# Performance work log

Hardware: AMD Instinct MI355X
Metric: run time of the kernel (lower is better)

## Reference

```python
import jax, jax.numpy as jnp
import numpy as np

N = 40000          # spots (nodes)
G = 3000           # genes (input features)
C = 20             # num_classes
E = N * 16         # edges (avg degree 16)


def _uniform(key, shape, stdv):
    return jax.random.uniform(key, shape, jnp.float32, -stdv, stdv)


def _linear_params(key, n_in, n_out):
    # torch Linear default init: U(-1/sqrt(in), 1/sqrt(in)); stored as [in, out]
    k1, k2 = jax.random.split(key)
    s = 1.0 / np.sqrt(n_in)
    return _uniform(k1, (n_in, n_out), s), _uniform(k2, (n_out,), s)


def setup_inputs() -> dict:
    key = jax.random.key(0)
    ks = jax.random.split(key, 32)
    x = jax.random.normal(ks[0], (N, G), jnp.float32)
    adj_rows = jax.random.randint(ks[1], (E,), 0, N, jnp.int32)
    adj_cols = jax.random.randint(ks[2], (E,), 0, N, jnp.int32)
    adj_vals = jax.random.uniform(ks[3], (E,), jnp.float32)

    # GCN weights: GraphConvolution init U(-1/sqrt(out), 1/sqrt(out)), no bias
    def gcn_w(k, fi, fo):
        return _uniform(k, (fi, fo), 1.0 / np.sqrt(fo))

    inp = {
        "x": x, "adj_rows": adj_rows, "adj_cols": adj_cols, "adj_vals": adj_vals,
        "W1": gcn_w(ks[4], G, 512), "W2": gcn_w(ks[5], 512, 256),
        "W3": gcn_w(ks[6], 256, 128), "W4": gcn_w(ks[7], 128, 128),
        "W5": gcn_w(ks[8], 128, C),
    }
    # AE linear layers
    for name, (fi, fo), k in [
        ("enc1", (G, 512), ks[9]), ("enc2", (512, 256), ks[10]),
        ("enc3", (256, 128), ks[11]), ("zl", (128, 128), ks[12]),
        ("dec1", (128, 128), ks[13]), ("dec2", (128, 256), ks[14]),
        ("dec3", (256, 512), ks[15]), ("xbar", (512, G), ks[16]),
    ]:
        w, b = _linear_params(k, fi, fo)
        inp[name + "_w"], inp[name + "_b"] = w, b
    # Attention projection vectors (Linear(in_size, 1, bias=False))
    inp["a1"] = _uniform(ks[17], (512,), 1.0 / np.sqrt(512))
    inp["a2"] = _uniform(ks[18], (256,), 1.0 / np.sqrt(256))
    inp["a3"] = _uniform(ks[19], (128,), 1.0 / np.sqrt(128))
    inp["a4"] = _uniform(ks[20], (128,), 1.0 / np.sqrt(128))
    inp["scale"] = jax.random.normal(ks[21], (G,), jnp.float32)
    inp["additive"] = jax.random.normal(ks[22], (G,), jnp.float32)
    return inp


def _spmm(rows, cols, vals, dense, n):
    # out[r] = sum_e vals[e] * dense[cols[e]] for rows[e]==r  (sparse [n,n] @ dense)
    return jax.ops.segment_sum(vals[:, None] * dense[cols], rows, num_segments=n)


def _gcn(x, rows, cols, vals, W, n, active=True):
    out = _spmm(rows, cols, vals, x @ W, n)
    return jax.nn.relu(out) if active else out


def _attn(h, t, a):
    # stack two [N,D] branches, softmax over the branch axis, weighted sum
    z = jnp.stack([h, t], axis=1)           # [N,2,D]
    w = jnp.einsum('nbd,d->nb', z, a)        # [N,2]
    beta = jax.nn.softmax(w, axis=1)
    return jnp.einsum('nb,nbd->nd', beta, z)


def reference(x, adj_rows, adj_cols, adj_vals,
              W1, W2, W3, W4, W5,
              enc1_w, enc1_b, enc2_w, enc2_b, enc3_w, enc3_b, zl_w, zl_b,
              dec1_w, dec1_b, dec2_w, dec2_b, dec3_w, dec3_b, xbar_w, xbar_b,
              a1, a2, a3, a4, scale, additive):
    n = x.shape[0]
    # autoencoder
    t1 = jax.nn.relu(x @ enc1_w + enc1_b)
    t2 = jax.nn.relu(t1 @ enc2_w + enc2_b)
    t3 = jax.nn.relu(t2 @ enc3_w + enc3_b)
    z = t3 @ zl_w + zl_b
    d1 = jax.nn.relu(z @ dec1_w + dec1_b)
    d2 = jax.nn.relu(d1 @ dec2_w + dec2_b)
    d3 = jax.nn.relu(d2 @ dec3_w + dec3_b)
    x_bar = d3 @ xbar_w + xbar_b
    # GCN stack with attention-fused AE skip connections
    h = _gcn(x, adj_rows, adj_cols, adj_vals, W1, n)
    emb = _attn(h, t1, a1)
    h = _gcn(emb, adj_rows, adj_cols, adj_vals, W2, n)
    emb = _attn(h, t2, a2)
    h = _gcn(emb, adj_rows, adj_cols, adj_vals, W3, n)
    emb = _attn(h, t3, a3)
    h = _gcn(emb, adj_rows, adj_cols, adj_vals, W4, n)
    emb = _attn(h, z, a4)
    output = _gcn(emb, adj_rows, adj_cols, adj_vals, W5, n, active=False)
    return output, x_bar, jax.nn.sigmoid(scale), jnp.exp(additive)
```

## Files before the change

### kernel.cpp

```cpp
#include <hip/hip_runtime.h>
#include <cmath>

typedef unsigned short u16;
typedef unsigned int u32;
typedef __attribute__((ext_vector_type(8))) short short8;
typedef __attribute__((ext_vector_type(4))) short short4v;
typedef __attribute__((ext_vector_type(4))) float f32x4;

__device__ __forceinline__ float bf2f(u16 h) {
  union { u32 u; float f; } v; v.u = ((u32)h) << 16; return v.f;
}
__device__ __forceinline__ u16 f2bf(float f) {
  union { float f; u32 u; } v; v.f = f;
  u32 u = v.u;
  u32 r = (u + 0x7FFFu + ((u >> 16) & 1u)) >> 16;
  return (u16)r;
}

__global__ void convx_kernel(const float* __restrict__ x, u16* __restrict__ A0) {
  int idx = blockIdx.x * 256 + threadIdx.x;
  int r = blockIdx.y;
  if (idx >= 752) return;
  short4v o;
  if (r < 40000 && idx < 750) {
    float4 v = *(const float4*)(x + (size_t)r * 3000 + idx * 4);
    o[0] = (short)f2bf(v.x); o[1] = (short)f2bf(v.y);
    o[2] = (short)f2bf(v.z); o[3] = (short)f2bf(v.w);
  } else {
    o[0] = 0; o[1] = 0; o[2] = 0; o[3] = 0;
  }
  *(short4v*)(A0 + (size_t)r * 3008 + idx * 4) = o;
}

__global__ void convw_kernel(const float* __restrict__ W, u16* __restrict__ Wt,
                             int K, int N, int Kp) {
  int k = blockIdx.x * 256 + threadIdx.x;
  int n = blockIdx.y;
  if (k >= Kp) return;
  float v = (k < K && n < N) ? W[(size_t)k * N + n] : 0.f;
  Wt[(size_t)n * Kp + k] = f2bf(v);
}

__global__ void zero_kernel(int* p, int n) {
  int i = blockIdx.x * 256 + threadIdx.x;
  if (i < n) p[i] = 0;
}
__global__ void count_kernel(const int* __restrict__ rows, int* __restrict__ counts, int E) {
  int i = blockIdx.x * 256 + threadIdx.x;
  if (i < E) atomicAdd(&counts[rows[i]], 1);
}
__global__ __launch_bounds__(1024) void scan_kernel(const int* __restrict__ counts,
                                                    int* __restrict__ rowptr,
                                                    int* __restrict__ cursor, int n) {
  __shared__ int buf[1024];
  __shared__ int carry_s;
  int tid = threadIdx.x;
  if (tid == 0) carry_s = 0;
  __syncthreads();
  for (int base = 0; base < n; base += 1024) {
    int i = base + tid;
    int v = (i < n) ? counts[i] : 0;
    buf[tid] = v;
    __syncthreads();
    for (int off = 1; off < 1024; off <<= 1) {
      int tv = (tid >= off) ? buf[tid - off] : 0;
      __syncthreads();
      buf[tid] += tv;
      __syncthreads();
    }
    int incl = buf[tid];
    int carry = carry_s;
    if (i < n) { int ex = carry + incl - v; rowptr[i] = ex; cursor[i] = ex; }
    __syncthreads();
    if (tid == 1023) carry_s = carry + incl;
    __syncthreads();
  }
  if (tid == 0) rowptr[n] = carry_s;
}
__global__ void scatter_kernel(const int* __restrict__ rows, const int* __restrict__ cols,
                               const float* __restrict__ vals, int* __restrict__ cursor,
                               int* __restrict__ cols_s, float* __restrict__ vals_s, int E) {
  int i = blockIdx.x * 256 + threadIdx.x;
  if (i < E) {
    int r = rows[i];
    int p = atomicAdd(&cursor[r], 1);
    cols_s[p] = cols[i];
    vals_s[p] = vals[i];
  }
}

#define BM 128
#define BN 128
#define BK 32

template <bool BIAS, bool RELU, bool OUTBF16, int CH>
__global__ __launch_bounds__(256, 2) void gemm_bf16(
    const u16* __restrict__ A, int lda, const u16* __restrict__ Bt, int ldb,
    void* __restrict__ C1, int ldc,
    const float* __restrict__ bias, int M, int Nreal, int K, int MT, int NT) {
  __shared__ __align__(16) u16 As[2][BM * BK];
  __shared__ __align__(16) u16 Bs[2][BN * BK];
  const int lin = blockIdx.x;
  const int per = CH * NT;
  const int g = lin / per;
  const int r0 = lin - g * per;
  const int bx0 = g * CH;
  const int cw = min(CH, MT - bx0);
  const int bx = bx0 + r0 % cw;
  const int by = r0 / cw;

  const int tid = threadIdx.x;
  const int lane = tid & 63;
  const int wave = tid >> 6;
  const int mblk = bx * BM;
  const int nblk = by * BN;
  const int wm = (wave & 1) * 64;
  const int wn = (wave >> 1) * 64;
  const int ml = lane & 15;
  const int kg = lane >> 4;

  f32x4 acc[4][4];
#pragma unroll
  for (int i = 0; i < 4; ++i)
#pragma unroll
    for (int j = 0; j < 4; ++j) acc[i][j] = (f32x4)(0.f);

  const int nk = K / BK;
  const int sr = tid >> 2;
  const int sc = (tid & 3) * 8;
  const u16* gA0 = A + (size_t)(mblk + sr) * lda + sc;
  const u16* gA1 = A + (size_t)(mblk + sr + 64) * lda + sc;
  const u16* gB0 = Bt + (size_t)(nblk + sr) * ldb + sc;
  const u16* gB1 = Bt + (size_t)(nblk + sr + 64) * ldb + sc;

  auto stage = [&](int buf, int kt) {
    const int ko = kt * BK;
    u16* lA = &As[buf][0] + wave * 512;
    u16* lB = &Bs[buf][0] + wave * 512;
    __builtin_amdgcn_global_load_lds((const void*)(gA0 + ko), (void*)lA, 16, 0, 0);
    __builtin_amdgcn_global_load_lds((const void*)(gA1 + ko), (void*)(lA + 2048), 16, 0, 0);
    __builtin_amdgcn_global_load_lds((const void*)(gB0 + ko), (void*)lB, 16, 0, 0);
    __builtin_amdgcn_global_load_lds((const void*)(gB1 + ko), (void*)(lB + 2048), 16, 0, 0);
  };

  stage(0, 0);
  asm volatile("s_waitcnt vmcnt(0)" ::: "memory");
  __syncthreads();

  int cur = 0;
  for (int kt = 0; kt < nk; ++kt) {
    if (kt + 1 < nk) stage(cur ^ 1, kt + 1);
    short8 af[4], bfr[4];
#pragma unroll
    for (int i = 0; i < 4; ++i) {
      af[i] = *(const short8*)&As[cur][(wm + i * 16 + ml) * BK + kg * 8];
      bfr[i] = *(const short8*)&Bs[cur][(wn + i * 16 + ml) * BK + kg * 8];
    }
#pragma unroll
    for (int i = 0; i < 4; ++i)
#pragma unroll
      for (int j = 0; j < 4; ++j)
        acc[i][j] = __builtin_amdgcn_mfma_f32_16x16x32_bf16(af[i], bfr[j], acc[i][j], 0, 0, 0);
    asm volatile("s_waitcnt vmcnt(0)" ::: "memory");
    __syncthreads();
    cur ^= 1;
  }

#pragma unroll
  for (int i = 0; i < 4; ++i) {
    const int row0 = mblk + wm + i * 16 + kg * 4;
#pragma unroll
    for (int j = 0; j < 4; ++j) {
      const int col = nblk + wn + j * 16 + ml;
      if (col < Nreal) {
        float bv = BIAS ? bias[col] : 0.f;
#pragma unroll
        for (int r = 0; r < 4; ++r) {
          const int row = row0 + r;
          if (row < M) {
            float v = acc[i][j][r] + bv;
            if (RELU) v = fmaxf(v, 0.f);
            if (OUTBF16)
              ((u16*)C1)[(size_t)row * ldc + col] = f2bf(v);
            else
              ((float*)C1)[(size_t)row * ldc + col] = v;
          }
        }
      }
    }
  }
}

template <bool BIAS, bool RELU, bool OUTBF16, bool SPLIT>
__global__ __launch_bounds__(512, 1) void gemm256v2(
    const u16* __restrict__ A, int lda, const u16* __restrict__ Bt, int ldb,
    void* __restrict__ C1, void* __restrict__ C2, int ldc,
    const float* __restrict__ bias, int M, int Nreal, int K, int MT, int NT) {
  __shared__ __align__(16) u16 smem[(2 * 128 + 2 * 256) * 64];
  u16* As0 = smem;
  u16* Bs0 = smem + 2 * 128 * 64;
  const int tid = threadIdx.x;
  const int lane = tid & 63;
  const int wave = tid >> 6;
  const int wm = wave >> 2;
  const int wn = wave & 3;
  const int ml = lane & 15;
  const int kg = lane >> 4;

  const int grp = blockIdx.x / (8 * NT);
  const int rr = blockIdx.x % (8 * NT);
  const int nb = min(8, MT - grp * 8);
  const int bx = grp * 8 + rr % nb;
  const int by = rr / nb;
  const int mblk = bx * 128;
  const int nblk = by * 256;

  f32x4 acc[4][4];
#pragma unroll
  for (int i = 0; i < 4; ++i)
#pragma unroll
    for (int j = 0; j < 4; ++j) acc[i][j] = (f32x4)(0.f);

  const int srow = tid >> 3;
  const int clog = (tid & 7) ^ (srow & 7);
  const size_t abase = (size_t)(mblk + srow) * lda + clog * 8;
  const size_t bbase = (size_t)(nblk + srow) * ldb + clog * 8;
  const int NKT = K / 64;

  auto stageA = [&](int d, int kt, int h) {
    u16* dst = As0 + d * 8192 + h * 4096 + wave * 512;
    const u16* src = A + abase + (size_t)h * 64 * lda + kt * 64;
    __builtin_amdgcn_global_load_lds((const void*)src, (void*)dst, 16, 0, 0);
  };
  auto stageB = [&](int d, int kt, int h) {
    u16* dst = Bs0 + d * 16384 + h * 4096 + wave * 512;
    const u16* src = Bt + bbase + (size_t)h * 64 * ldb + kt * 64;
    __builtin_amdgcn_global_load_lds((const void*)src, (void*)dst, 16, 0, 0);
  };
  auto stageAll = [&](int d, int kt) {
    stageB(d, kt, 0); stageB(d, kt, 1); stageB(d, kt, 2); stageB(d, kt, 3);
    stageA(d, kt, 0); stageA(d, kt, 1);
  };
  auto readA = [&](int d, int im, int kk) -> short8 {
    const int r = wm * 64 + im * 16 + ml;
    const int ch = (kk * 4 + kg) ^ (r & 7);
    return *(const short8*)&As0[d * 8192 + r * 64 + ch * 8];
  };
  auto readB = [&](int d, int j, int kk) -> short8 {
    const int r = wn * 64 + j * 16 + ml;
    const int ch = (kk * 4 + kg) ^ (r & 7);
    return *(const short8*)&Bs0[d * 16384 + r * 64 + ch * 8];
  };

  stageAll(0, 0);
  __syncthreads();

  for (int kt = 0; kt < NKT; ++kt) {
    const int d = kt & 1;
    if (kt + 1 < NKT) stageAll(d ^ 1, kt + 1);

    short8 b[4][2];
#pragma unroll
    for (int j = 0; j < 4; ++j) { b[j][0] = readB(d, j, 0); b[j][1] = readB(d, j, 1); }
    short8 aC0k0 = readA(d, 0, 0), aC0k1 = readA(d, 0, 1);
    short8 aC1k0 = readA(d, 1, 0), aC1k1 = readA(d, 1, 1);
#pragma unroll
    for (int q = 0; q < 2; ++q) {
      short8 aN0k0, aN0k1, aN1k0, aN1k1;
      if (q == 0) {
        aN0k0 = readA(d, 2, 0); aN0k1 = readA(d, 2, 1);
        aN1k0 = readA(d, 3, 0); aN1k1 = readA(d, 3, 1);
      }
      __builtin_amdgcn_s_setprio(1);
#pragma unroll
      for (int j = 0; j < 4; ++j) {
        acc[2 * q][j]     = __builtin_amdgcn_mfma_f32_16x16x32_bf16(aC0k0, b[j][0], acc[2 * q][j], 0, 0, 0);
        acc[2 * q + 1][j] = __builtin_amdgcn_mfma_f32_16x16x32_bf16(aC1k0, b[j][0], acc[2 * q + 1][j], 0, 0, 0);
      }
#pragma unroll
      for (int j = 0; j < 4; ++j) {
        acc[2 * q][j]     = __builtin_amdgcn_mfma_f32_16x16x32_bf16(aC0k1, b[j][1], acc[2 * q][j], 0, 0, 0);
        acc[2 * q + 1][j] = __builtin_amdgcn_mfma_f32_16x16x32_bf16(aC1k1, b[j][1], acc[2 * q + 1][j], 0, 0, 0);
      }
      __builtin_amdgcn_s_setprio(0);
      if (q == 0) { aC0k0 = aN0k0; aC0k1 = aN0k1; aC1k0 = aN1k0; aC1k1 = aN1k1; }
    }
    __syncthreads();
  }

  if (!SPLIT && !OUTBF16) {
    float* ep = (float*)smem;
    const int ES = 260;
    const int scol = nblk + lane * 4;
    float bv0 = 0.f, bv1 = 0.f, bv2 = 0.f, bv3 = 0.f;
    if (BIAS) {
      if (scol + 3 < Nreal) {
        float4 b4 = *(const float4*)(bias + scol);
        bv0 = b4.x; bv1 = b4.y; bv2 = b4.z; bv3 = b4.w;
      } else {
        if (scol + 0 < Nreal) bv0 = bias[scol + 0];
        if (scol + 1 < Nreal) bv1 = bias[scol + 1];
        if (scol + 2 < Nreal) bv2 = bias[scol + 2];
        if (scol + 3 < Nreal) bv3 = bias[scol + 3];
      }
    }
#pragma unroll
    for (int p = 0; p < 2; ++p) {
      if (p) __syncthreads();
#pragma unroll
      for (int il = 0; il < 2; ++il) {
        const int i = 2 * p + il;
        const int lrow0 = wm * 32 + il * 16 + kg * 4;
#pragma unroll
        for (int j = 0; j < 4; ++j) {
          const int colL = wn * 64 + j * 16 + ml;
#pragma unroll
          for (int r = 0; r < 4; ++r) ep[(lrow0 + r) * ES + colL] = acc[i][j][r];
        }
      }
      __syncthreads();
#pragma unroll
      for (int it = 0; it < 8; ++it) {
        const int lrow = wave * 8 + it;
        const int grow = mblk + p * 32 + (lrow & 31) + (lrow >> 5) * 64;
        if (grow < M) {
          float v0 = ep[lrow * ES + lane * 4 + 0] + bv0;
          float v1 = ep[lrow * ES + lane * 4 + 1] + bv1;
          float v2 = ep[lrow * ES + lane * 4 + 2] + bv2;
          float v3 = ep[lrow * ES + lane * 4 + 3] + bv3;
          if (RELU) {
            v0 = fmaxf(v0, 0.f); v1 = fmaxf(v1, 0.f);
            v2 = fmaxf(v2, 0.f); v3 = fmaxf(v3, 0.f);
          }
          float* dst = (float*)C1 + (size_t)grow * ldc + scol;
          if (scol + 3 < Nreal) {
            float4 v; v.x = v0; v.y = v1; v.z = v2; v.w = v3;
            *(float4*)dst = v;
          } else {
            if (scol + 0 < Nreal) dst[0] = v0;
            if (scol + 1 < Nreal) dst[1] = v1;
            if (scol + 2 < Nreal) dst[2] = v2;
            if (scol + 3 < Nreal) dst[3] = v3;
          }
        }
      }
    }
    return;
  }

  const int crow0 = mblk + wm * 64;
  const int ccol0 = nblk + wn * 64;
#pragma unroll
  for (int i = 0; i < 4; ++i) {
    const int row0 = crow0 + i * 16 + kg * 4;
#pragma unroll
    for (int j = 0; j < 4; ++j) {
      const int col = ccol0 + j * 16 + ml;
      if (SPLIT) {
        const bool second = (nblk >= 512);
        const float bv = second ? 0.f : bias[col];
#pragma unroll
        for (int r = 0; r < 4; ++r) {
          const int row = row0 + r;
          if (row < M) {
            float v = acc[i][j][r] + bv;
            if (!second) v = fmaxf(v, 0.f);
            u16* dst = second ? (u16*)C2 : (u16*)C1;
            dst[(size_t)row * 512 + (second ? col - 512 : col)] = f2bf(v);
          }
        }
      } else if (col < Nreal) {
        const float bv = BIAS ? bias[col] : 0.f;
#pragma unroll
        for (int r = 0; r < 4; ++r) {
          const int row = row0 + r;
          if (row < M) {
            float v = acc[i][j][r] + bv;
            if (RELU) v = fmaxf(v, 0.f);
            if (OUTBF16)
              ((u16*)C1)[(size_t)row * ldc + col] = f2bf(v);
            else
              ((float*)C1)[(size_t)row * ldc + col] = v;
          }
        }
      }
    }
  }
}

template <int D>
__global__ __launch_bounds__(256) void spmm_attn(const int* __restrict__ rowptr,
                                                 const int* __restrict__ colidx,
                                                 const float* __restrict__ vals,
                                                 const u16* __restrict__ X,
                                                 const u16* __restrict__ T,
                                                 const float* __restrict__ a,
                                                 u16* __restrict__ emb) {
  constexpr int VE = D / 64;
  const int wave = threadIdx.x >> 6, lane = threadIdx.x & 63;
  const int row = blockIdx.x * 4 + wave;
  const int co = lane * VE;
  float h[VE];
#pragma unroll
  for (int j = 0; j < VE; ++j) h[j] = 0.f;
  const int s = rowptr[row], e = rowptr[row + 1];
  for (int i = s; i < e; ++i) {
    const int c = colidx[i];
    const float v = vals[i];
    const u16* xr = X + (size_t)c * D + co;
    if constexpr (VE == 8) {
      short8 x8 = *(const short8*)xr;
#pragma unroll
      for (int j = 0; j < 8; ++j) h[j] += v * bf2f((u16)x8[j]);
    } else if constexpr (VE == 4) {
      short4v x4 = *(const short4v*)xr;
#pragma unroll
      for (int j = 0; j < 4; ++j) h[j] += v * bf2f((u16)x4[j]);
    } else {
      u32 x2 = *(const u32*)xr;
      h[0] += v * bf2f((u16)(x2 & 0xffffu));
      h[1] += v * bf2f((u16)(x2 >> 16));
    }
  }
#pragma unroll
  for (int j = 0; j < VE; ++j) h[j] = fmaxf(h[j], 0.f);

  float tv[VE];
  const u16* tr = T + (size_t)row * D + co;
  if constexpr (VE == 8) {
    short8 t8 = *(const short8*)tr;
#pragma unroll
    for (int j = 0; j < 8; ++j) tv[j] = bf2f((u16)t8[j]);
  } else if constexpr (VE == 4) {
    short4v t4 = *(const short4v*)tr;
#pragma unroll
    for (int j = 0; j < 4; ++j) tv[j] = bf2f((u16)t4[j]);
  } else {
    u32 t2 = *(const u32*)tr;
    tv[0] = bf2f((u16)(t2 & 0xffffu)); tv[1] = bf2f((u16)(t2 >> 16));
  }

  float wh = 0.f, wt = 0.f;
#pragma unroll
  for (int j = 0; j < VE; ++j) {
    float av = a[co + j];
    wh += av * h[j];
    wt += av * tv[j];
  }
  for (int off = 32; off; off >>= 1) {
    wh += __shfl_xor(wh, off);
    wt += __shfl_xor(wt, off);
  }
  float m = fmaxf(wh, wt);
  float e1 = expf(wh - m), e2 = expf(wt - m);
  float inv = 1.f / (e1 + e2);
  float b1 = e1 * inv, b2 = e2 * inv;
  u16* er = emb + (size_t)row * D + co;
  if constexpr (VE == 8) {
    short8 o;
#pragma unroll
    for (int j = 0; j < 8; ++j) o[j] = (short)f2bf(b1 * h[j] + b2 * tv[j]);
    *(short8*)er = o;
  } else if constexpr (VE == 4) {
    short4v o;
#pragma unroll
    for (int j = 0; j < 4; ++j) o[j] = (short)f2bf(b1 * h[j] + b2 * tv[j]);
    *(short4v*)er = o;
  } else {
    *(u32*)er = (u32)f2bf(b1 * h[0] + b2 * tv[0]) | ((u32)f2bf(b1 * h[1] + b2 * tv[1]) << 16);
  }
}

__global__ __launch_bounds__(64) void spmm_out_kernel(const int* __restrict__ rowptr,
                                                      const int* __restrict__ colidx,
                                                      const float* __restrict__ vals,
                                                      const u16* __restrict__ X,
                                                      float* __restrict__ Y) {
  int row = blockIdx.x;
  int c = threadIdx.x;
  float acc = 0.f;
  int s = rowptr[row], e = rowptr[row + 1];
  for (int i = s; i < e; ++i) {
    int col = colidx[i];
    float v = vals[i];
    if (c < 20) acc += v * bf2f(X[(size_t)col * 20 + c]);
  }
  if (c < 20) Y[(size_t)row * 20 + c] = acc;
}

__global__ __launch_bounds__(64) void xw5_kernel(const u16* __restrict__ emb,
                                                 const float* __restrict__ W5,
                                                 u16* __restrict__ xw5) {
  int row = blockIdx.x;
  int c = threadIdx.x;
  if (c >= 20) return;
  const short8* er = (const short8*)(emb + (size_t)row * 128);
  float acc = 0.f;
#pragma unroll
  for (int k8 = 0; k8 < 16; ++k8) {
    short8 v = er[k8];
#pragma unroll
    for (int j = 0; j < 8; ++j) acc += bf2f((u16)v[j]) * W5[(k8 * 8 + j) * 20 + c];
  }
  xw5[(size_t)row * 20 + c] = f2bf(acc);
}

__global__ void sig_exp_kernel(const float* __restrict__ scale, const float* __restrict__ additive,
                               float* __restrict__ osig, float* __restrict__ oexp, int g) {
  int i = blockIdx.x * 256 + threadIdx.x;
  if (i < g) {
    osig[i] = 1.f / (1.f + expf(-scale[i]));
    oexp[i] = expf(additive[i]);
  }
}

extern "C" void kernel_launch(void* const* d_in, const int* in_sizes, int n_in,
                              void* d_out, int out_size, void* d_ws, size_t ws_size,
                              hipStream_t stream) {
  (void)n_in; (void)out_size; (void)ws_size;
  const float* x      = (const float*)d_in[0];
  const int*   arows  = (const int*)d_in[1];
  const int*   acols  = (const int*)d_in[2];
  const float* avals  = (const float*)d_in[3];
  const float* W1     = (const float*)d_in[4];
  const float* W2     = (const float*)d_in[5];
  const float* W3     = (const float*)d_in[6];
  const float* W4     = (const float*)d_in[7];
  const float* W5     = (const float*)d_in[8];
  const float* enc1_w = (const float*)d_in[9],  *enc1_b = (const float*)d_in[10];
  const float* enc2_w = (const float*)d_in[11], *enc2_b = (const float*)d_in[12];
  const float* enc3_w = (const float*)d_in[13], *enc3_b = (const float*)d_in[14];
  const float* zl_w   = (const float*)d_in[15], *zl_b   = (const float*)d_in[16];
  const float* dec1_w = (const float*)d_in[17], *dec1_b = (const float*)d_in[18];
  const float* dec2_w = (const float*)d_in[19], *dec2_b = (const float*)d_in[20];
  const float* dec3_w = (const float*)d_in[21], *dec3_b = (const float*)d_in[22];
  const float* xbar_w = (const float*)d_in[23], *xbar_b = (const float*)d_in[24];
  const float* a1 = (const float*)d_in[25], *a2 = (const float*)d_in[26];
  const float* a3 = (const float*)d_in[27], *a4 = (const float*)d_in[28];
  const float* scale = (const float*)d_in[29], *additive = (const float*)d_in[30];

  const int E = in_sizes[1];
  const int N = 40000, G = 3000, Kx = 3008;
  const int Mp = 40192;

  float* out      = (float*)d_out;
  float* out_gcn  = out;
  float* out_xbar = out + (size_t)N * 20;
  float* out_sig  = out_xbar + (size_t)N * G;
  float* out_exp  = out_sig + G;

  char* wsb = (char*)d_ws;
  size_t off = 0;
  auto alloc = [&](size_t b) -> void* {
    void* p = wsb + off;
    off = (off + b + 255) & ~(size_t)255;
    return p;
  };
  u16* A0    = (u16*)alloc((size_t)Mp * Kx * 2);
  u16* t1    = (u16*)alloc((size_t)Mp * 512 * 2);
  u16* t2    = (u16*)alloc((size_t)Mp * 256 * 2);
  u16* t3    = (u16*)alloc((size_t)Mp * 128 * 2);
  u16* zb    = (u16*)alloc((size_t)Mp * 128 * 2);
  u16* dd1   = (u16*)alloc((size_t)Mp * 128 * 2);
  u16* dd2   = (u16*)alloc((size_t)Mp * 256 * 2);
  u16* dd3   = (u16*)alloc((size_t)Mp * 512 * 2);
  u16* xw    = (u16*)alloc((size_t)Mp * 512 * 2);
  u16* emb   = (u16*)alloc((size_t)Mp * 512 * 2);
  u16* xw5   = (u16*)alloc((size_t)N * 20 * 2);
  u16* catT  = (u16*)alloc((size_t)1024 * Kx * 2);
  u16* enc2T = (u16*)alloc((size_t)256 * 512 * 2);
  u16* enc3T = (u16*)alloc((size_t)128 * 256 * 2);
  u16* zlT   = (u16*)alloc((size_t)128 * 128 * 2);
  u16* dec1T = (u16*)alloc((size_t)128 * 128 * 2);
  u16* dec2T = (u16*)alloc((size_t)256 * 128 * 2);
  u16* dec3T = (u16*)alloc((size_t)512 * 256 * 2);
  u16* xbarT = (u16*)alloc((size_t)3072 * 512 * 2);
  u16* W2T   = (u16*)alloc((size_t)256 * 512 * 2);
  u16* W3T   = (u16*)alloc((size_t)128 * 256 * 2);
  u16* W4T   = (u16*)alloc((size_t)128 * 128 * 2);
  int* counts = (int*)alloc((size_t)N * 4);
  int* rowptr = (int*)alloc((size_t)(N + 1) * 4);
  int* cursor = (int*)alloc((size_t)N * 4);
  int* colss  = (int*)alloc((size_t)E * 4);
  float* valss = (float*)alloc((size_t)E * 4);

  convx_kernel<<<dim3(3, Mp), 256, 0, stream>>>(x, A0);
  auto convw = [&](const float* W, u16* Wt, int K, int Nw, int Kp, int Np) {
    convw_kernel<<<dim3((Kp + 255) / 256, Np), 256, 0, stream>>>(W, Wt, K, Nw, Kp);
  };
  convw(enc1_w, catT,             3000, 512, Kx, 512);
  convw(W1,     catT + 512 * Kx,  3000, 512, Kx, 512);
  convw(enc2_w, enc2T, 512, 256, 512, 256);
  convw(enc3_w, enc3T, 256, 128, 256, 128);
  convw(zl_w,   zlT,   128, 128, 128, 128);
  convw(dec1_w, dec1T, 128, 128, 128, 128);
  convw(dec2_w, dec2T, 128, 256, 128, 256);
  convw(dec3_w, dec3T, 256, 512, 256, 512);
  convw(xbar_w, xbarT, 512, 3000, 512, 3072);
  convw(W2,     W2T,   512, 256, 512, 256);
  convw(W3,     W3T,   256, 128, 256, 128);
  convw(W4,     W4T,   128, 128, 128, 128);

  zero_kernel<<<(N + 255) / 256, 256, 0, stream>>>(counts, N);
  count_kernel<<<(E + 255) / 256, 256, 0, stream>>>(arows, counts, E);
  scan_kernel<<<1, 1024, 0, stream>>>(counts, rowptr, cursor, N);
  scatter_kernel<<<(E + 255) / 256, 256, 0, stream>>>(arows, acols, avals, cursor, colss, valss, E);

  const int MT = 313;
  gemm256v2<false, false, true, true><<<MT * 4, 512, 0, stream>>>(
      A0, Kx, catT, Kx, t1, xw, 512, enc1_b, N, 1024, Kx, MT, 4);
  gemm_bf16<true, true, true, 32><<<MT * 2, 256, 0, stream>>>(
      t1, 512, enc2T, 512, t2, 256, enc2_b, N, 256, 512, MT, 2);
  gemm_bf16<true, true, true, 32><<<MT * 1, 256, 0, stream>>>(
      t2, 256, enc3T, 256, t3, 128, enc3_b, N, 128, 256, MT, 1);
  gemm_bf16<true, false, true, 32><<<MT * 1, 256, 0, stream>>>(
      t3, 128, zlT, 128, zb, 128, zl_b, N, 128, 128, MT, 1);
  gemm_bf16<true, true, true, 32><<<MT * 1, 256, 0, stream>>>(
      zb, 128, dec1T, 128, dd1, 128, dec1_b, N, 128, 128, MT, 1);
  gemm_bf16<true, true, true, 32><<<MT * 2, 256, 0, stream>>>(
      dd1, 128, dec2T, 128, dd2, 256, dec2_b, N, 256, 128, MT, 2);
  gemm_bf16<true, true, true, 32><<<MT * 4, 256, 0, stream>>>(
      dd2, 256, dec3T, 256, dd3, 512, dec3_b, N, 512, 256, MT, 4);
  gemm256v2<true, false, false, false><<<MT * 12, 512, 0, stream>>>(
      dd3, 512, xbarT, 512, out_xbar, nullptr, 3000, xbar_b, N, 3000, 512, MT, 12);

  spmm_attn<512><<<N / 4, 256, 0, stream>>>(rowptr, colss, valss, xw, t1, a1, emb);
  gemm_bf16<false, false, true, 32><<<MT * 2, 256, 0, stream>>>(
      emb, 512, W2T, 512, xw, 256, nullptr, N, 256, 512, MT, 2);
  spmm_attn<256><<<N / 4, 256, 0, stream>>>(rowptr, colss, valss, xw, t2, a2, emb);
  gemm_bf16<false, false, true, 32><<<MT * 1, 256, 0, stream>>>(
      emb, 256, W3T, 256, xw, 128, nullptr, N, 128, 256, MT, 1);
  spmm_attn<128><<<N / 4, 256, 0, stream>>>(rowptr, colss, valss, xw, t3, a3, emb);
  gemm_bf16<false, false, true, 32><<<MT * 1, 256, 0, stream>>>(
      emb, 128, W4T, 128, xw, 128, nullptr, N, 128, 128, MT, 1);
  spmm_attn<128><<<N / 4, 256, 0, stream>>>(rowptr, colss, valss, xw, zb, a4, emb);

  xw5_kernel<<<N, 64, 0, stream>>>(emb, W5, xw5);
  spmm_out_kernel<<<N, 64, 0, stream>>>(rowptr, colss, valss, xw5, out_gcn);

  sig_exp_kernel<<<(G + 255) / 256, 256, 0, stream>>>(scale, additive, out_sig, out_exp, G);
}
```

Baseline: 1.464 ms.

## Enlarge big GEMM tiles to 256x256 with staggered staging and partial waitcnt

Replaces the 128x256 tile GEMM with a 256x256 tile variant used for the fused enc1/W1 GEMM and the x_bar GEMM. Each wave now covers 128 rows, which halves B-tile reloads per output. The next K-tile's global-to-LDS loads are split into four chunks placed between MFMA groups, with explicit vmcnt waits and raw barriers in place of full __syncthreads. The split bf16 output for the first GEMM now goes through the LDS epilogue with vectorized stores. The cost is twice the accumulator registers and LDS, and fewer blocks (157 row tiles), which may leave CUs idle at the tail.

Result: faster. 1.380 ms (-5.7%).

```diff
diff --git a/kernel.cpp b/kernel.cpp
--- a/kernel.cpp
+++ b/kernel.cpp
@@ -191,14 +191,12 @@
   }
 }
 
-template <bool BIAS, bool RELU, bool OUTBF16, bool SPLIT>
-__global__ __launch_bounds__(512, 1) void gemm256v2(
+template <int MODE>
+__global__ __launch_bounds__(512, 1) void gemm256p(
     const u16* __restrict__ A, int lda, const u16* __restrict__ Bt, int ldb,
     void* __restrict__ C1, void* __restrict__ C2, int ldc,
-    const float* __restrict__ bias, int M, int Nreal, int K, int MT, int NT) {
-  __shared__ __align__(16) u16 smem[(2 * 128 + 2 * 256) * 64];
-  u16* As0 = smem;
-  u16* Bs0 = smem + 2 * 128 * 64;
+    const float* __restrict__ bias, int M, int Nreal, int K, int MT2, int NT) {
+  __shared__ __align__(16) u16 smem[2 * 2 * 256 * 64];
   const int tid = threadIdx.x;
   const int lane = tid & 63;
   const int wave = tid >> 6;
@@ -209,15 +207,15 @@
 
   const int grp = blockIdx.x / (8 * NT);
   const int rr = blockIdx.x % (8 * NT);
-  const int nb = min(8, MT - grp * 8);
+  const int nb = min(8, MT2 - grp * 8);
   const int bx = grp * 8 + rr % nb;
   const int by = rr / nb;
-  const int mblk = bx * 128;
+  const int mblk = bx * 256;
   const int nblk = by * 256;
 
-  f32x4 acc[4][4];
-#pragma unroll
-  for (int i = 0; i < 4; ++i)
+  f32x4 acc[8][4];
+#pragma unroll
+  for (int i = 0; i < 8; ++i)
 #pragma unroll
     for (int j = 0; j < 4; ++j) acc[i][j] = (f32x4)(0.f);
 
@@ -228,89 +226,143 @@
   const int NKT = K / 64;
 
   auto stageA = [&](int d, int kt, int h) {
-    u16* dst = As0 + d * 8192 + h * 4096 + wave * 512;
+    u16* dst = smem + d * 16384 + h * 4096 + wave * 512;
     const u16* src = A + abase + (size_t)h * 64 * lda + kt * 64;
     __builtin_amdgcn_global_load_lds((const void*)src, (void*)dst, 16, 0, 0);
   };
   auto stageB = [&](int d, int kt, int h) {
-    u16* dst = Bs0 + d * 16384 + h * 4096 + wave * 512;
+    u16* dst = smem + 32768 + d * 16384 + h * 4096 + wave * 512;
     const u16* src = Bt + bbase + (size_t)h * 64 * ldb + kt * 64;
     __builtin_amdgcn_global_load_lds((const void*)src, (void*)dst, 16, 0, 0);
   };
-  auto stageAll = [&](int d, int kt) {
-    stageB(d, kt, 0); stageB(d, kt, 1); stageB(d, kt, 2); stageB(d, kt, 3);
-    stageA(d, kt, 0); stageA(d, kt, 1);
-  };
+  auto stageU0 = [&](int d, int kt) { stageB(d, kt, 0); stageB(d, kt, 1); };
+  auto stageU1 = [&](int d, int kt) { stageB(d, kt, 2); stageB(d, kt, 3); };
+  auto stageU2 = [&](int d, int kt) { stageA(d, kt, 0); stageA(d, kt, 2); };
+  auto stageU3 = [&](int d, int kt) { stageA(d, kt, 1); stageA(d, kt, 3); };
   auto readA = [&](int d, int im, int kk) -> short8 {
-    const int r = wm * 64 + im * 16 + ml;
+    const int r = wm * 128 + im * 16 + ml;
     const int ch = (kk * 4 + kg) ^ (r & 7);
-    return *(const short8*)&As0[d * 8192 + r * 64 + ch * 8];
+    return *(const short8*)&smem[d * 16384 + r * 64 + ch * 8];
   };
   auto readB = [&](int d, int j, int kk) -> short8 {
     const int r = wn * 64 + j * 16 + ml;
     const int ch = (kk * 4 + kg) ^ (r & 7);
-    return *(const short8*)&Bs0[d * 16384 + r * 64 + ch * 8];
+    return *(const short8*)&smem[32768 + d * 16384 + r * 64 + ch * 8];
   };
 
-  stageAll(0, 0);
-  __syncthreads();
+  stageU0(0, 0); stageU1(0, 0); stageU2(0, 0); stageU3(0, 0);
+  asm volatile("s_waitcnt vmcnt(2)" ::: "memory");
+  __builtin_amdgcn_s_barrier();
 
   for (int kt = 0; kt < NKT; ++kt) {
     const int d = kt & 1;
-    if (kt + 1 < NKT) stageAll(d ^ 1, kt + 1);
-
+    const bool more = (kt + 1 < NKT);
     short8 b[4][2];
 #pragma unroll
     for (int j = 0; j < 4; ++j) { b[j][0] = readB(d, j, 0); b[j][1] = readB(d, j, 1); }
-    short8 aC0k0 = readA(d, 0, 0), aC0k1 = readA(d, 0, 1);
-    short8 aC1k0 = readA(d, 1, 0), aC1k1 = readA(d, 1, 1);
-#pragma unroll
-    for (int q = 0; q < 2; ++q) {
-      short8 aN0k0, aN0k1, aN1k0, aN1k1;
-      if (q == 0) {
-        aN0k0 = readA(d, 2, 0); aN0k1 = readA(d, 2, 1);
-        aN1k0 = readA(d, 3, 0); aN1k1 = readA(d, 3, 1);
-      }
+    {
+      short8 a00 = readA(d, 0, 0), a01 = readA(d, 0, 1);
+      short8 a10 = readA(d, 1, 0), a11 = readA(d, 1, 1);
+      if (more) stageU0(d ^ 1, kt + 1);
       __builtin_amdgcn_s_setprio(1);
 #pragma unroll
       for (int j = 0; j < 4; ++j) {
-        acc[2 * q][j]     = __builtin_amdgcn_mfma_f32_16x16x32_bf16(aC0k0, b[j][0], acc[2 * q][j], 0, 0, 0);
-        acc[2 * q + 1][j] = __builtin_amdgcn_mfma_f32_16x16x32_bf16(aC1k0, b[j][0], acc[2 * q + 1][j], 0, 0, 0);
-      }
-#pragma unroll
-      for (int j = 0; j < 4; ++j) {
-        acc[2 * q][j]     = __builtin_amdgcn_mfma_f32_16x16x32_bf16(aC0k1, b[j][1], acc[2 * q][j], 0, 0, 0);
-        acc[2 * q + 1][j] = __builtin_amdgcn_mfma_f32_16x16x32_bf16(aC1k1, b[j][1], acc[2 * q + 1][j], 0, 0, 0);
+        acc[0][j] = __builtin_amdgcn_mfma_f32_16x16x32_bf16(a00, b[j][0], acc[0][j], 0, 0, 0);
+        acc[1][j] = __builtin_amdgcn_mfma_f32_16x16x32_bf16(a10, b[j][0], acc[1][j], 0, 0, 0);
+      }
+#pragma unroll
+      for (int j = 0; j < 4; ++j) {
+        acc[0][j] = __builtin_amdgcn_mfma_f32_16x16x32_bf16(a01, b[j][1], acc[0][j], 0, 0, 0);
+        acc[1][j] = __builtin_amdgcn_mfma_f32_16x16x32_bf16(a11, b[j][1], acc[1][j], 0, 0, 0);
       }
       __builtin_amdgcn_s_setprio(0);
-      if (q == 0) { aC0k0 = aN0k0; aC0k1 = aN0k1; aC1k0 = aN1k0; aC1k1 = aN1k1; }
-    }
-    __syncthreads();
-  }
-
-  if (!SPLIT && !OUTBF16) {
-    float* ep = (float*)smem;
-    const int ES = 260;
-    const int scol = nblk + lane * 4;
-    float bv0 = 0.f, bv1 = 0.f, bv2 = 0.f, bv3 = 0.f;
-    if (BIAS) {
-      if (scol + 3 < Nreal) {
-        float4 b4 = *(const float4*)(bias + scol);
-        bv0 = b4.x; bv1 = b4.y; bv2 = b4.z; bv3 = b4.w;
-      } else {
-        if (scol + 0 < Nreal) bv0 = bias[scol + 0];
-        if (scol + 1 < Nreal) bv1 = bias[scol + 1];
-        if (scol + 2 < Nreal) bv2 = bias[scol + 2];
-        if (scol + 3 < Nreal) bv3 = bias[scol + 3];
-      }
-    }
-#pragma unroll
-    for (int p = 0; p < 2; ++p) {
-      if (p) __syncthreads();
-#pragma unroll
-      for (int il = 0; il < 2; ++il) {
-        const int i = 2 * p + il;
-        const int lrow0 = wm * 32 + il * 16 + kg * 4;
+    }
+    {
+      short8 a00 = readA(d, 2, 0), a01 = readA(d, 2, 1);
+      short8 a10 = readA(d, 3, 0), a11 = readA(d, 3, 1);
+      if (more) stageU1(d ^ 1, kt + 1);
+      __builtin_amdgcn_s_setprio(1);
+#pragma unroll
+      for (int j = 0; j < 4; ++j) {
+        acc[2][j] = __builtin_amdgcn_mfma_f32_16x16x32_bf16(a00, b[j][0], acc[2][j], 0, 0, 0);
+        acc[3][j] = __builtin_amdgcn_mfma_f32_16x16x32_bf16(a10, b[j][0], acc[3][j], 0, 0, 0);
+      }
+#pragma unroll
+      for (int j = 0; j < 4; ++j) {
+        acc[2][j] = __builtin_amdgcn_mfma_f32_16x16x32_bf16(a01, b[j][1], acc[2][j], 0, 0, 0);
+        acc[3][j] = __builtin_amdgcn_mfma_f32_16x16x32_bf16(a11, b[j][1], acc[3][j], 0, 0, 0);
+      }
+      __builtin_amdgcn_s_setprio(0);
+    }
+    if (more) asm volatile("s_waitcnt vmcnt(4)" ::: "memory");
+    else      asm volatile("s_waitcnt vmcnt(0)" ::: "memory");
+    __builtin_amdgcn_s_barrier();
+    {
+      short8 a00 = readA(d, 4, 0), a01 = readA(d, 4, 1);
+      short8 a10 = readA(d, 5, 0), a11 = readA(d, 5, 1);
+      if (more) stageU2(d ^ 1, kt + 1);
+      __builtin_amdgcn_s_setprio(1);
+#pragma unroll
+      for (int j = 0; j < 4; ++j) {
+        acc[4][j] = __builtin_amdgcn_mfma_f32_16x16x32_bf16(a00, b[j][0], acc[4][j], 0, 0, 0);
+        acc[5][j] = __builtin_amdgcn_mfma_f32_16x16x32_bf16(a10, b[j][0], acc[5][j], 0, 0, 0);
+      }
+#pragma unroll
+      for (int j = 0; j < 4; ++j) {
+        acc[4][j] = __builtin_amdgcn_mfma_f32_16x16x32_bf16(a01, b[j][1], acc[4][j], 0, 0, 0);
+        acc[5][j] = __builtin_amdgcn_mfma_f32_16x16x32_bf16(a11, b[j][1], acc[5][j], 0, 0, 0);
+      }
+      __builtin_amdgcn_s_setprio(0);
+    }
+    {
+      short8 a00 = readA(d, 6, 0), a01 = readA(d, 6, 1);
+      short8 a10 = readA(d, 7, 0), a11 = readA(d, 7, 1);
+      if (more) stageU3(d ^ 1, kt + 1);
+      __builtin_amdgcn_s_setprio(1);
+#pragma unroll
+      for (int j = 0; j < 4; ++j) {
+        acc[6][j] = __builtin_amdgcn_mfma_f32_16x16x32_bf16(a00, b[j][0], acc[6][j], 0, 0, 0);
+        acc[7][j] = __builtin_amdgcn_mfma_f32_16x16x32_bf16(a10, b[j][0], acc[7][j], 0, 0, 0);
+      }
+#pragma unroll
+      for (int j = 0; j < 4; ++j) {
+        acc[6][j] = __builtin_amdgcn_mfma_f32_16x16x32_bf16(a01, b[j][1], acc[6][j], 0, 0, 0);
+        acc[7][j] = __builtin_amdgcn_mfma_f32_16x16x32_bf16(a11, b[j][1], acc[7][j], 0, 0, 0);
+      }
+      __builtin_amdgcn_s_setprio(0);
+    }
+    if (more) asm volatile("s_waitcnt vmcnt(2)" ::: "memory");
+    __builtin_amdgcn_s_barrier();
+  }
+
+  __syncthreads();
+
+  float* ep = (float*)smem;
+  const int ES = 260;
+  const int colg = nblk + lane * 4;
+  const bool second = (MODE == 0) && (nblk >= 512);
+  float bv0 = 0.f, bv1 = 0.f, bv2 = 0.f, bv3 = 0.f;
+  if (MODE == 0) {
+    if (!second) { float4 b4 = *(const float4*)(bias + colg); bv0 = b4.x; bv1 = b4.y; bv2 = b4.z; bv3 = b4.w; }
+  } else {
+    if (colg + 3 < Nreal) {
+      float4 b4 = *(const float4*)(bias + colg);
+      bv0 = b4.x; bv1 = b4.y; bv2 = b4.z; bv3 = b4.w;
+    } else {
+      if (colg + 0 < Nreal) bv0 = bias[colg + 0];
+      if (colg + 1 < Nreal) bv1 = bias[colg + 1];
+      if (colg + 2 < Nreal) bv2 = bias[colg + 2];
+      if (colg + 3 < Nreal) bv3 = bias[colg + 3];
+    }
+  }
+#pragma unroll
+  for (int p = 0; p < 4; ++p) {
+    if (p) __syncthreads();
+    if (wm == (p >> 1)) {
+#pragma unroll
+      for (int ii = 0; ii < 4; ++ii) {
+        const int i = (p & 1) * 4 + ii;
+        const int lrow0 = ii * 16 + kg * 4;
 #pragma unroll
         for (int j = 0; j < 4; ++j) {
           const int colL = wn * 64 + j * 16 + ml;
@@ -318,69 +370,34 @@
           for (int r = 0; r < 4; ++r) ep[(lrow0 + r) * ES + colL] = acc[i][j][r];
         }
       }
-      __syncthreads();
-#pragma unroll
-      for (int it = 0; it < 8; ++it) {
-        const int lrow = wave * 8 + it;
-        const int grow = mblk + p * 32 + (lrow & 31) + (lrow >> 5) * 64;
-        if (grow < M) {
-          float v0 = ep[lrow * ES + lane * 4 + 0] + bv0;
-          float v1 = ep[lrow * ES + lane * 4 + 1] + bv1;
-          float v2 = ep[lrow * ES + lane * 4 + 2] + bv2;
-          float v3 = ep[lrow * ES + lane * 4 + 3] + bv3;
-          if (RELU) {
-            v0 = fmaxf(v0, 0.f); v1 = fmaxf(v1, 0.f);
-            v2 = fmaxf(v2, 0.f); v3 = fmaxf(v3, 0.f);
-          }
-          float* dst = (float*)C1 + (size_t)grow * ldc + scol;
-          if (scol + 3 < Nreal) {
+    }
+    __syncthreads();
+#pragma unroll
+    for (int it = 0; it < 8; ++it) {
+      const int lrow = wave * 8 + it;
+      const int grow = mblk + p * 64 + lrow;
+      if (grow < M) {
+        float v0 = ep[lrow * ES + lane * 4 + 0] + bv0;
+        float v1 = ep[lrow * ES + lane * 4 + 1] + bv1;
+        float v2 = ep[lrow * ES + lane * 4 + 2] + bv2;
+        float v3 = ep[lrow * ES + lane * 4 + 3] + bv3;
+        if (MODE == 0) {
+          if (!second) { v0 = fmaxf(v0, 0.f); v1 = fmaxf(v1, 0.f); v2 = fmaxf(v2, 0.f); v3 = fmaxf(v3, 0.f); }
+          u16* dst = (second ? (u16*)C2 : (u16*)C1) + (size_t)grow * 512 + (second ? colg - 512 : colg);
+          short4v o;
+          o[0] = (short)f2bf(v0); o[1] = (short)f2bf(v1);
+          o[2] = (short)f2bf(v2); o[3] = (short)f2bf(v3);
+          *(short4v*)dst = o;
+        } else {
+          float* dst = (float*)C1 + (size_t)grow * ldc + colg;
+          if (colg + 3 < Nreal) {
             float4 v; v.x = v0; v.y = v1; v.z = v2; v.w = v3;
             *(float4*)dst = v;
           } else {
-            if (scol + 0 < Nreal) dst[0] = v0;
-            if (scol + 1 < Nreal) dst[1] = v1;
-            if (scol + 2 < Nreal) dst[2] = v2;
-            if (scol + 3 < Nreal) dst[3] = v3;
-          }
-        }
-      }
-    }
-    return;
-  }
-
-  const int crow0 = mblk + wm * 64;
-  const int ccol0 = nblk + wn * 64;
-#pragma unroll
-  for (int i = 0; i < 4; ++i) {
-    const int row0 = crow0 + i * 16 + kg * 4;
-#pragma unroll
-    for (int j = 0; j < 4; ++j) {
-      const int col = ccol0 + j * 16 + ml;
-      if (SPLIT) {
-        const bool second = (nblk >= 512);
-        const float bv = second ? 0.f : bias[col];
-#pragma unroll
-        for (int r = 0; r < 4; ++r) {
-          const int row = row0 + r;
-          if (row < M) {
-            float v = acc[i][j][r] + bv;
-            if (!second) v = fmaxf(v, 0.f);
-            u16* dst = second ? (u16*)C2 : (u16*)C1;
-            dst[(size_t)row * 512 + (second ? col - 512 : col)] = f2bf(v);
-          }
-        }
-      } else if (col < Nreal) {
-        const float bv = BIAS ? bias[col] : 0.f;
-#pragma unroll
-        for (int r = 0; r < 4; ++r) {
-          const int row = row0 + r;
-          if (row < M) {
-            float v = acc[i][j][r] + bv;
-            if (RELU) v = fmaxf(v, 0.f);
-            if (OUTBF16)
-              ((u16*)C1)[(size_t)row * ldc + col] = f2bf(v);
-            else
-              ((float*)C1)[(size_t)row * ldc + col] = v;
+            if (colg + 0 < Nreal) dst[0] = v0;
+            if (colg + 1 < Nreal) dst[1] = v1;
+            if (colg + 2 < Nreal) dst[2] = v2;
+            if (colg + 3 < Nreal) dst[3] = v3;
           }
         }
       }
@@ -607,8 +624,9 @@
   scatter_kernel<<<(E + 255) / 256, 256, 0, stream>>>(arows, acols, avals, cursor, colss, valss, E);
 
   const int MT = 313;
-  gemm256v2<false, false, true, true><<<MT * 4, 512, 0, stream>>>(
-      A0, Kx, catT, Kx, t1, xw, 512, enc1_b, N, 1024, Kx, MT, 4);
+  const int MT2 = 157;
+  gemm256p<0><<<MT2 * 4, 512, 0, stream>>>(
+      A0, Kx, catT, Kx, t1, xw, 512, enc1_b, N, 1024, Kx, MT2, 4);
   gemm_bf16<true, true, true, 32><<<MT * 2, 256, 0, stream>>>(
       t1, 512, enc2T, 512, t2, 256, enc2_b, N, 256, 512, MT, 2);
   gemm_bf16<true, true, true, 32><<<MT * 1, 256, 0, stream>>>(
@@ -621,8 +639,8 @@
       dd1, 128, dec2T, 128, dd2, 256, dec2_b, N, 256, 128, MT, 2);
   gemm_bf16<true, true, true, 32><<<MT * 4, 256, 0, stream>>>(
       dd2, 256, dec3T, 256, dd3, 512, dec3_b, N, 512, 256, MT, 4);
-  gemm256v2<true, false, false, false><<<MT * 12, 512, 0, stream>>>(
-      dd3, 512, xbarT, 512, out_xbar, nullptr, 3000, xbar_b, N, 3000, 512, MT, 12);
+  gemm256p<1><<<MT2 * 12, 512, 0, stream>>>(
+      dd3, 512, xbarT, 512, out_xbar, nullptr, 3000, xbar_b, N, 3000, 512, MT2, 12);
 
   spmm_attn<512><<<N / 4, 256, 0, stream>>>(rowptr, colss, valss, xw, t1, a1, emb);
   gemm_bf16<false, false, true, 32><<<MT * 2, 256, 0, stream>>>(
```
